# Kernel optimization log

Measured on AMD Instinct MI355X. Metric: run time of the kernel, lower is better.

The kernel has to match this reference:

```python
import jax, jax.numpy as jnp
import numpy as np

EMBED_DIM = 2048
NUM_HEADS = 16
LATENT_DIM = 512
HEAD_DIM = EMBED_DIM // NUM_HEADS


def setup_inputs() -> dict:
    key = jax.random.key(0)
    ks = jax.random.split(key, 9)
    s = 0.02
    x = jax.random.normal(ks[0], (2, 2048, EMBED_DIM), dtype=jnp.float32)
    # torch Linear weights stored as [out, in]
    q_w = jax.random.normal(ks[1], (EMBED_DIM, EMBED_DIM), jnp.float32) * s
    q_b = jax.random.normal(ks[2], (EMBED_DIM,), jnp.float32) * s
    kvd_w = jax.random.normal(ks[3], (LATENT_DIM, EMBED_DIM), jnp.float32) * s
    kvd_b = jax.random.normal(ks[4], (LATENT_DIM,), jnp.float32) * s
    kvu_w = jax.random.normal(ks[5], (EMBED_DIM * 2, LATENT_DIM), jnp.float32) * s
    kvu_b = jax.random.normal(ks[6], (EMBED_DIM * 2,), jnp.float32) * s
    out_w = jax.random.normal(ks[7], (EMBED_DIM, EMBED_DIM), jnp.float32) * s
    out_b = jax.random.normal(ks[8], (EMBED_DIM,), jnp.float32) * s
    return {"x": x, "q_w": q_w, "q_b": q_b, "kvd_w": kvd_w, "kvd_b": kvd_b,
            "kvu_w": kvu_w, "kvu_b": kvu_b, "out_w": out_w, "out_b": out_b}


def reference(x, q_w, q_b, kvd_w, kvd_b, kvu_w, kvu_b, out_w, out_b):
    b, s, _ = x.shape
    q = x @ q_w.T + q_b                      # [b,s,E]
    latent = x @ kvd_w.T + kvd_b             # [b,s,L]
    kv = latent @ kvu_w.T + kvu_b            # [b,s,2E]
    k, v = kv[..., :EMBED_DIM], kv[..., EMBED_DIM:]
    def heads(t):
        return t.reshape(b, s, NUM_HEADS, HEAD_DIM).transpose(0, 2, 1, 3)  # [b,h,s,d]
    qh, kh, vh = heads(q), heads(k), heads(v)
    scores = jnp.einsum('bhqd,bhkd->bhqk', qh, kh) / jnp.sqrt(jnp.float32(HEAD_DIM))
    attn = jax.nn.softmax(scores, axis=-1)
    out = jnp.einsum('bhqk,bhkd->bhqd', attn, vh)
    out = out.transpose(0, 2, 1, 3).reshape(b, s, EMBED_DIM)
    return out @ out_w.T + out_b
```

## Files before the change

kernel.cpp:

```cpp
#include <hip/hip_runtime.h>

typedef unsigned short u16;
typedef __attribute__((ext_vector_type(8))) __bf16 bf16x8;
typedef __attribute__((ext_vector_type(8))) unsigned short u16x8;
typedef __attribute__((ext_vector_type(4))) float f32x4;
typedef __attribute__((ext_vector_type(16))) float f32x16;

#define BK 32
#define TILE_ELEMS (128 * BK)
#define QSCALE 0.12753706518066536f

#if __has_builtin(__builtin_amdgcn_exp2f)
#define EXP2(x) __builtin_amdgcn_exp2f(x)
#else
#define EXP2(x) exp2f(x)
#endif

__device__ __forceinline__ u16 f32_to_bf16(float f) {
  __bf16 h = (__bf16)f;
  return __builtin_bit_cast(u16, h);
}

__device__ __forceinline__ void gll16(const u16* g, u16* l) {
  __builtin_amdgcn_global_load_lds(
      (const __attribute__((address_space(1))) void*)g,
      (__attribute__((address_space(3))) void*)l, 16, 0, 0);
}

__device__ __forceinline__ void xcd_swz(int& bn, int& bm) {
  const int nx = gridDim.x;
  const int nwg = nx * gridDim.y;
  const int wg = blockIdx.y * nx + blockIdx.x;
  const int cpx = nwg >> 3;
  const int swz = (wg & 7) * cpx + (wg >> 3);
  bn = swz % nx;
  bm = swz / nx;
}

__global__ __launch_bounds__(256) void cvt_all(
    const float* __restrict__ x, const float* __restrict__ qw,
    const float* __restrict__ kvdw, const float* __restrict__ kvuw,
    const float* __restrict__ outw, u16* __restrict__ X, u16* __restrict__ W1,
    u16* __restrict__ W2, u16* __restrict__ W3, u16* __restrict__ W4) {
  int blk = blockIdx.x;
  const float* src;
  u16* dst;
  int base;
  if (blk < 8192)       { src = x;    dst = X;  base = blk; }
  else if (blk < 12288) { src = qw;   dst = W1; base = blk - 8192; }
  else if (blk < 13312) { src = kvdw; dst = W2; base = blk - 12288; }
  else if (blk < 15360) { src = kvuw; dst = W3; base = blk - 13312; }
  else                  { src = outw; dst = W4; base = blk - 15360; }
  int i = base * 1024 + threadIdx.x * 4;
  float4 v = *(const float4*)(src + i);
  ushort4 o;
  o.x = f32_to_bf16(v.x);
  o.y = f32_to_bf16(v.y);
  o.z = f32_to_bf16(v.z);
  o.w = f32_to_bf16(v.w);
  *(ushort4*)(dst + i) = o;
}

__device__ __forceinline__ void gemm_core(const u16* __restrict__ A_tile,
                                          const u16* __restrict__ B_tile, int K,
                                          u16* As, u16* Bs, f32x4 acc[4][4]) {
  const int tid = threadIdx.x;
  const int w = tid >> 6, lane = tid & 63;
  const int wm = (w >> 1) << 6, wn = (w & 1) << 6;
  const int quad = lane >> 4, l15 = lane & 15;

  const u16* Ap = A_tile + (tid >> 2) * K + (tid & 3) * 8;
  const u16* Bp = B_tile + (tid >> 2) * K + (tid & 3) * 8;
  u16* Asw = As + w * 512;
  u16* Bsw = Bs + w * 512;

  gll16(Ap, Asw);
  gll16(Ap + 64 * K, Asw + 2048);
  gll16(Bp, Bsw);
  gll16(Bp + 64 * K, Bsw + 2048);

  int p = 0;
  for (int k0 = 0; k0 < K; k0 += BK) {
    const int kn = k0 + BK;
    __syncthreads();
    if (kn < K) {
      const int off = (p ^ 1) * TILE_ELEMS;
      gll16(Ap + kn, Asw + off);
      gll16(Ap + 64 * K + kn, Asw + off + 2048);
      gll16(Bp + kn, Bsw + off);
      gll16(Bp + 64 * K + kn, Bsw + off + 2048);
    }
    const u16* Asr = As + p * TILE_ELEMS;
    const u16* Bsr = Bs + p * TILE_ELEMS;
    bf16x8 af[4], bf[4];
#pragma unroll
    for (int i = 0; i < 4; i++)
      af[i] = *(const bf16x8*)(Asr + (wm + i * 16 + l15) * BK + quad * 8);
#pragma unroll
    for (int j = 0; j < 4; j++)
      bf[j] = *(const bf16x8*)(Bsr + (wn + j * 16 + l15) * BK + quad * 8);
#pragma unroll
    for (int i = 0; i < 4; i++)
#pragma unroll
      for (int j = 0; j < 4; j++)
        acc[i][j] =
            __builtin_amdgcn_mfma_f32_16x16x32_bf16(af[i], bf[j], acc[i][j], 0, 0, 0);
    p ^= 1;
  }
}

__global__ __launch_bounds__(256) void gemm_qlat(const u16* __restrict__ X,
                                                 const u16* __restrict__ QW,
                                                 const u16* __restrict__ KVDW,
                                                 const float* __restrict__ q_b,
                                                 const float* __restrict__ kvd_b,
                                                 u16* __restrict__ Qb,
                                                 u16* __restrict__ Lat) {
  __shared__ __align__(16) u16 As[2 * TILE_ELEMS];
  __shared__ __align__(16) u16 Bs[2 * TILE_ELEMS];
  int bn, bm;
  xcd_swz(bn, bm);
  const bool isq = bn < 16;
  const u16* B_tile = isq ? QW + (size_t)bn * 128 * 2048
                          : KVDW + (size_t)(bn - 16) * 128 * 2048;
  f32x4 acc[4][4];
  const f32x4 z = {0.f, 0.f, 0.f, 0.f};
#pragma unroll
  for (int i = 0; i < 4; i++)
#pragma unroll
    for (int j = 0; j < 4; j++) acc[i][j] = z;
  gemm_core(X + (size_t)bm * 128 * 2048, B_tile, 2048, As, Bs, acc);

  const float* bias = isq ? q_b : kvd_b;
  u16* C = isq ? Qb : Lat;
  const int N = isq ? 2048 : 512;
  const float scale = isq ? QSCALE : 1.0f;
  const int colbase = (isq ? bn : bn - 16) * 128;

  const int tid = threadIdx.x;
  const int w = tid >> 6, lane = tid & 63;
  const int wm = (w >> 1) << 6, wn = (w & 1) << 6;
  const int quad = lane >> 4, l15 = lane & 15;
  const int row0 = bm * 128 + wm + quad * 4;
  const int col0 = colbase + wn + l15;
#pragma unroll
  for (int i = 0; i < 4; i++)
#pragma unroll
    for (int j = 0; j < 4; j++) {
      int col = col0 + j * 16;
      float bv = bias[col];
#pragma unroll
      for (int r = 0; r < 4; r++) {
        int row = row0 + i * 16 + r;
        C[(size_t)row * N + col] = f32_to_bf16((acc[i][j][r] + bv) * scale);
      }
    }
}

__global__ __launch_bounds__(256) void gemm_f32out(const u16* __restrict__ A,
                                                   const u16* __restrict__ B,
                                                   const float* __restrict__ bias,
                                                   float* __restrict__ C, int K, int N) {
  __shared__ __align__(16) u16 As[2 * TILE_ELEMS];
  __shared__ __align__(16) u16 Bs[2 * TILE_ELEMS];
  int bn, bm;
  xcd_swz(bn, bm);
  f32x4 acc[4][4];
  const f32x4 z = {0.f, 0.f, 0.f, 0.f};
#pragma unroll
  for (int i = 0; i < 4; i++)
#pragma unroll
    for (int j = 0; j < 4; j++) acc[i][j] = z;
  gemm_core(A + (size_t)bm * 128 * K, B + (size_t)bn * 128 * K, K, As, Bs, acc);

  const int tid = threadIdx.x;
  const int w = tid >> 6, lane = tid & 63;
  const int wm = (w >> 1) << 6, wn = (w & 1) << 6;
  const int quad = lane >> 4, l15 = lane & 15;
  const int row0 = bm * 128 + wm + quad * 4;
  const int col0 = bn * 128 + wn + l15;
#pragma unroll
  for (int i = 0; i < 4; i++)
#pragma unroll
    for (int j = 0; j < 4; j++) {
      int col = col0 + j * 16;
      float bv = bias[col];
#pragma unroll
      for (int r = 0; r < 4; r++) {
        int row = row0 + i * 16 + r;
        C[(size_t)row * N + col] = acc[i][j][r] + bv;
      }
    }
}

__global__ __launch_bounds__(256) void gemm_kv(const u16* __restrict__ A,
                                               const u16* __restrict__ B,
                                               const float* __restrict__ bias,
                                               u16* __restrict__ Khat,
                                               u16* __restrict__ Vt, int K) {
  __shared__ __align__(16) u16 As[2 * TILE_ELEMS];
  __shared__ __align__(16) u16 Bs[2 * TILE_ELEMS];
  int bn, bm;
  xcd_swz(bn, bm);
  f32x4 acc[4][4];
  const f32x4 z = {0.f, 0.f, 0.f, 0.f};
#pragma unroll
  for (int i = 0; i < 4; i++)
#pragma unroll
    for (int j = 0; j < 4; j++) acc[i][j] = z;
  gemm_core(A + (size_t)bm * 128 * K, B + (size_t)bn * 128 * K, K, As, Bs, acc);

  const int tid = threadIdx.x;
  const int w = tid >> 6, lane = tid & 63;
  const int wm = (w >> 1) << 6, wn = (w & 1) << 6;
  const int quad = lane >> 4, l15 = lane & 15;
  const int row0 = bm * 128 + wm + quad * 4;
  const int col0 = bn * 128 + wn + l15;
#pragma unroll
  for (int i = 0; i < 4; i++)
#pragma unroll
    for (int j = 0; j < 4; j++) {
      int n = col0 + j * 16;
      float bv = bias[n];
#pragma unroll
      for (int r = 0; r < 4; r++) {
        int row = row0 + i * 16 + r;
        int bb = row >> 11, s = row & 2047;
        u16 val = f32_to_bf16(acc[i][j][r] + bv);
        if (n < 2048) {
          int h = n >> 7, d = n & 127;
          Khat[((size_t)(bb * 16 + h) * 2048 + s) * 128 + d] = val;
        } else {
          int h = (n - 2048) >> 7, d = n & 127;
          Vt[((size_t)(bb * 16 + h) * 128 + d) * 2048 + s] = val;
        }
      }
    }
}

__global__ __launch_bounds__(256) void attn_kernel(const u16* __restrict__ Q,
                                                   const u16* __restrict__ Khat,
                                                   const u16* __restrict__ Vt,
                                                   u16* __restrict__ O) {
  __shared__ __align__(16) u16 Ks[2][32 * 136];
  __shared__ __align__(16) u16 Vs[2][128 * 40];

  const int tid = threadIdx.x;
  const int w = tid >> 6, lane = tid & 63;
  const int l31 = lane & 31, half = lane >> 5;
  const int qt = blockIdx.x & 15;
  const int h = (blockIdx.x >> 4) & 15;
  const int b = blockIdx.x >> 8;
  const int bh = b * 16 + h;

  bf16x8 qf[8];
  {
    const u16* qrow = Q + (size_t)(b * 2048 + qt * 128 + w * 32 + l31) * 2048 +
                      h * 128 + half * 8;
#pragma unroll
    for (int kc = 0; kc < 8; kc++) qf[kc] = *(const bf16x8*)(qrow + kc * 16);
  }

  f32x16 oacc[4];
#pragma unroll
  for (int nt = 0; nt < 4; nt++)
#pragma unroll
    for (int r = 0; r < 16; r++) oacc[nt][r] = 0.f;
  float ls0 = 0.f, ls1 = 0.f, ls2 = 0.f, ls3 = 0.f;

  const u16* Kg = Khat + (size_t)bh * 2048 * 128;
  const u16* Vg = Vt + (size_t)bh * 128 * 2048;

  const int kkr = tid >> 4, kc0 = tid & 15;
  const int vd = tid >> 2, vc0 = tid & 3;
  const int vlo = (vc0 >> 1) * 16 + (vc0 & 1) * 4;
  const int vhi = vlo + 8;

  u16x8 kv[2], vv[2];
#pragma unroll
  for (int it = 0; it < 2; it++) {
    kv[it] = *(const u16x8*)(Kg + (size_t)(kkr + it * 16) * 128 + kc0 * 8);
    vv[it] = *(const u16x8*)(Vg + (size_t)(vd + it * 64) * 2048 + vc0 * 8);
  }
#pragma unroll
  for (int it = 0; it < 2; it++) {
    *(u16x8*)(Ks[0] + (kkr + it * 16) * 136 + kc0 * 8) = kv[it];
    const unsigned long long* vp = (const unsigned long long*)&vv[it];
    *(unsigned long long*)(Vs[0] + (vd + it * 64) * 40 + vlo) = vp[0];
    *(unsigned long long*)(Vs[0] + (vd + it * 64) * 40 + vhi) = vp[1];
  }

  int p = 0;
  for (int key0 = 0; key0 < 2048; key0 += 32) {
    const int kn = (key0 + 32 < 2048) ? (key0 + 32) : 0;
#pragma unroll
    for (int it = 0; it < 2; it++) {
      kv[it] = *(const u16x8*)(Kg + (size_t)(kn + kkr + it * 16) * 128 + kc0 * 8);
      vv[it] = *(const u16x8*)(Vg + (size_t)(vd + it * 64) * 2048 + kn + vc0 * 8);
    }
    __syncthreads();

    f32x16 sacc;
#pragma unroll
    for (int r = 0; r < 16; r++) sacc[r] = 0.f;
#pragma unroll
    for (int kc = 0; kc < 8; kc++) {
      bf16x8 kf = *(const bf16x8*)(Ks[p] + l31 * 136 + kc * 16 + half * 8);
      sacc = __builtin_amdgcn_mfma_f32_32x32x16_bf16(kf, qf[kc], sacc, 0, 0, 0);
    }

    float e[16];
#pragma unroll
    for (int r = 0; r < 16; r++) e[r] = EXP2(sacc[r]);
    ls0 += e[0] + e[4] + e[8] + e[12];
    ls1 += e[1] + e[5] + e[9] + e[13];
    ls2 += e[2] + e[6] + e[10] + e[14];
    ls3 += e[3] + e[7] + e[11] + e[15];
    bf16x8 pa0, pa1;
#pragma unroll
    for (int i = 0; i < 8; i++) {
      pa0[i] = (__bf16)e[i];
      pa1[i] = (__bf16)e[8 + i];
    }

#pragma unroll
    for (int nt = 0; nt < 4; nt++) {
      bf16x8 vf0 = *(const bf16x8*)(Vs[p] + (nt * 32 + l31) * 40 + half * 8);
      bf16x8 vf1 = *(const bf16x8*)(Vs[p] + (nt * 32 + l31) * 40 + 16 + half * 8);
      oacc[nt] = __builtin_amdgcn_mfma_f32_32x32x16_bf16(pa0, vf0, oacc[nt], 0, 0, 0);
      oacc[nt] = __builtin_amdgcn_mfma_f32_32x32x16_bf16(pa1, vf1, oacc[nt], 0, 0, 0);
    }

    const int pn = p ^ 1;
#pragma unroll
    for (int it = 0; it < 2; it++) {
      *(u16x8*)(Ks[pn] + (kkr + it * 16) * 136 + kc0 * 8) = kv[it];
      const unsigned long long* vp = (const unsigned long long*)&vv[it];
      *(unsigned long long*)(Vs[pn] + (vd + it * 64) * 40 + vlo) = vp[0];
      *(unsigned long long*)(Vs[pn] + (vd + it * 64) * 40 + vhi) = vp[1];
    }
    p = pn;
  }

  float lsum = (ls0 + ls1) + (ls2 + ls3);
  lsum += __shfl_xor(lsum, 32);
  float inv = 1.0f / lsum;
  float wr[16];
#pragma unroll
  for (int r = 0; r < 16; r++) {
    int ridx = (r & 3) + 8 * (r >> 2) + 4 * half;
    wr[r] = __shfl(inv, ridx);
  }

#pragma unroll
  for (int nt = 0; nt < 4; nt++)
#pragma unroll
    for (int r = 0; r < 16; r++) {
      int ridx = (r & 3) + 8 * (r >> 2) + 4 * half;
      int row = b * 2048 + qt * 128 + w * 32 + ridx;
      int col = h * 128 + nt * 32 + l31;
      O[(size_t)row * 2048 + col] = f32_to_bf16(oacc[nt][r] * wr[r]);
    }
}

extern "C" void kernel_launch(void* const* d_in, const int* in_sizes, int n_in,
                              void* d_out, int out_size, void* d_ws, size_t ws_size,
                              hipStream_t stream) {
  (void)in_sizes; (void)n_in; (void)out_size; (void)ws_size;
  const float* x     = (const float*)d_in[0];
  const float* q_w   = (const float*)d_in[1];
  const float* q_b   = (const float*)d_in[2];
  const float* kvd_w = (const float*)d_in[3];
  const float* kvd_b = (const float*)d_in[4];
  const float* kvu_w = (const float*)d_in[5];
  const float* kvu_b = (const float*)d_in[6];
  const float* out_w = (const float*)d_in[7];
  const float* out_b = (const float*)d_in[8];
  float* out = (float*)d_out;

  char* p = (char*)d_ws;
  u16* X    = (u16*)(p + 0);
  u16* W1   = (u16*)(p + (size_t)16 * 1024 * 1024);
  u16* W2   = (u16*)(p + (size_t)24 * 1024 * 1024);
  u16* W3   = (u16*)(p + (size_t)26 * 1024 * 1024);
  u16* W4   = (u16*)(p + (size_t)30 * 1024 * 1024);
  u16* Qb   = (u16*)(p + (size_t)38 * 1024 * 1024);
  u16* Lat  = (u16*)(p + (size_t)54 * 1024 * 1024);
  u16* Khat = (u16*)(p + (size_t)58 * 1024 * 1024);
  u16* Vt   = (u16*)(p + (size_t)74 * 1024 * 1024);
  u16* AO   = (u16*)(p + (size_t)90 * 1024 * 1024);

  cvt_all<<<dim3(19456), dim3(256), 0, stream>>>(x, q_w, kvd_w, kvu_w, out_w,
                                                 X, W1, W2, W3, W4);
  gemm_qlat<<<dim3(20, 32), dim3(256), 0, stream>>>(X, W1, W2, q_b, kvd_b, Qb, Lat);
  gemm_kv<<<dim3(32, 32), dim3(256), 0, stream>>>(Lat, W3, kvu_b, Khat, Vt, 512);
  attn_kernel<<<dim3(512), dim3(256), 0, stream>>>(Qb, Khat, Vt, AO);
  gemm_f32out<<<dim3(16, 32), dim3(256), 0, stream>>>(AO, W4, out_b, out, 2048, 2048);
}
```

Measured before the change: 364.0 us.

## Load K tiles directly to LDS with XOR swizzle, add block swizzle and setprio

K tiles in the attention kernel now travel from global memory straight into LDS through global_load_lds. The layout moves from padded rows to an XOR-swizzled unpadded one, and the read addressing is swizzled to match. This removes the register staging and the ds_write traffic for K and frees registers. The block index is also remapped so neighbouring blocks spread across batch and head, and s_setprio raises wave priority around the MFMA sections. One risk is that the direct loads now write the next buffer right after the barrier with no wait before the next iteration, so correctness depends on the existing barrier and vmcnt handling.

```diff
diff --git a/kernel.cpp b/kernel.cpp
--- a/kernel.cpp
+++ b/kernel.cpp
@@ -242,15 +242,17 @@
                                                    const u16* __restrict__ Khat,
                                                    const u16* __restrict__ Vt,
                                                    u16* __restrict__ O) {
-  __shared__ __align__(16) u16 Ks[2][32 * 136];
+  __shared__ __align__(16) u16 Ks[2 * 32 * 128];
   __shared__ __align__(16) u16 Vs[2][128 * 40];
 
   const int tid = threadIdx.x;
   const int w = tid >> 6, lane = tid & 63;
   const int l31 = lane & 31, half = lane >> 5;
-  const int qt = blockIdx.x & 15;
-  const int h = (blockIdx.x >> 4) & 15;
-  const int b = blockIdx.x >> 8;
+  const int idx = blockIdx.x;
+  const int swz = (idx & 7) * 64 + (idx >> 3);
+  const int qt = swz & 15;
+  const int h = (swz >> 4) & 15;
+  const int b = swz >> 8;
   const int bh = b * 16 + h;
 
   bf16x8 qf[8];
@@ -271,20 +273,31 @@
   const u16* Kg = Khat + (size_t)bh * 2048 * 128;
   const u16* Vg = Vt + (size_t)bh * 128 * 2048;
 
-  const int kkr = tid >> 4, kc0 = tid & 15;
+  int koff0, koff1;
+  {
+    const int P0 = w * 2048 + lane * 16;
+    const int r0 = P0 >> 8;
+    const int lin0 = P0 ^ ((r0 & 7) << 4);
+    koff0 = r0 * 128 + ((lin0 & 255) >> 1);
+    const int P1 = P0 + 1024;
+    const int r1 = P1 >> 8;
+    const int lin1 = P1 ^ ((r1 & 7) << 4);
+    koff1 = r1 * 128 + ((lin1 & 255) >> 1);
+  }
+  const int kx = (l31 & 7) << 3;
+
   const int vd = tid >> 2, vc0 = tid & 3;
   const int vlo = (vc0 >> 1) * 16 + (vc0 & 1) * 4;
   const int vhi = vlo + 8;
 
-  u16x8 kv[2], vv[2];
+  gll16(Kg + koff0, Ks + w * 1024);
+  gll16(Kg + koff1, Ks + w * 1024 + 512);
+  u16x8 vv[2];
+#pragma unroll
+  for (int it = 0; it < 2; it++)
+    vv[it] = *(const u16x8*)(Vg + (size_t)(vd + it * 64) * 2048 + vc0 * 8);
 #pragma unroll
   for (int it = 0; it < 2; it++) {
-    kv[it] = *(const u16x8*)(Kg + (size_t)(kkr + it * 16) * 128 + kc0 * 8);
-    vv[it] = *(const u16x8*)(Vg + (size_t)(vd + it * 64) * 2048 + vc0 * 8);
-  }
-#pragma unroll
-  for (int it = 0; it < 2; it++) {
-    *(u16x8*)(Ks[0] + (kkr + it * 16) * 136 + kc0 * 8) = kv[it];
     const unsigned long long* vp = (const unsigned long long*)&vv[it];
     *(unsigned long long*)(Vs[0] + (vd + it * 64) * 40 + vlo) = vp[0];
     *(unsigned long long*)(Vs[0] + (vd + it * 64) * 40 + vhi) = vp[1];
@@ -294,20 +307,24 @@
   for (int key0 = 0; key0 < 2048; key0 += 32) {
     const int kn = (key0 + 32 < 2048) ? (key0 + 32) : 0;
 #pragma unroll
-    for (int it = 0; it < 2; it++) {
-      kv[it] = *(const u16x8*)(Kg + (size_t)(kn + kkr + it * 16) * 128 + kc0 * 8);
+    for (int it = 0; it < 2; it++)
       vv[it] = *(const u16x8*)(Vg + (size_t)(vd + it * 64) * 2048 + kn + vc0 * 8);
-    }
     __syncthreads();
+    const int pn = p ^ 1;
+    gll16(Kg + kn * 128 + koff0, Ks + pn * 4096 + w * 1024);
+    gll16(Kg + kn * 128 + koff1, Ks + pn * 4096 + w * 1024 + 512);
 
     f32x16 sacc;
 #pragma unroll
     for (int r = 0; r < 16; r++) sacc[r] = 0.f;
+    const u16* Kr = Ks + p * 4096 + l31 * 128;
+    __builtin_amdgcn_s_setprio(1);
 #pragma unroll
     for (int kc = 0; kc < 8; kc++) {
-      bf16x8 kf = *(const bf16x8*)(Ks[p] + l31 * 136 + kc * 16 + half * 8);
+      bf16x8 kf = *(const bf16x8*)(Kr + ((kc * 16 + half * 8) ^ kx));
       sacc = __builtin_amdgcn_mfma_f32_32x32x16_bf16(kf, qf[kc], sacc, 0, 0, 0);
     }
+    __builtin_amdgcn_s_setprio(0);
 
     float e[16];
 #pragma unroll
@@ -323,6 +340,7 @@
       pa1[i] = (__bf16)e[8 + i];
     }
 
+    __builtin_amdgcn_s_setprio(1);
 #pragma unroll
     for (int nt = 0; nt < 4; nt++) {
       bf16x8 vf0 = *(const bf16x8*)(Vs[p] + (nt * 32 + l31) * 40 + half * 8);
@@ -330,11 +348,10 @@
       oacc[nt] = __builtin_amdgcn_mfma_f32_32x32x16_bf16(pa0, vf0, oacc[nt], 0, 0, 0);
       oacc[nt] = __builtin_amdgcn_mfma_f32_32x32x16_bf16(pa1, vf1, oacc[nt], 0, 0, 0);
     }
-
-    const int pn = p ^ 1;
+    __builtin_amdgcn_s_setprio(0);
+
 #pragma unroll
     for (int it = 0; it < 2; it++) {
-      *(u16x8*)(Ks[pn] + (kkr + it * 16) * 136 + kc0 * 8) = kv[it];
       const unsigned long long* vp = (const unsigned long long*)&vv[it];
       *(unsigned long long*)(Vs[pn] + (vd + it * 64) * 40 + vlo) = vp[0];
       *(unsigned long long*)(Vs[pn] + (vd + it * 64) * 40 + vhi) = vp[1];
```

New measurement: 369.7 us. About the same (+1.6%).
